# Performance work log

Measured on AMD Instinct MI355X. Metric: run time of the kernel, lower is better.

Reference implementation:

```python
import jax, jax.numpy as jnp
import numpy as np
from jax import lax

S = 20      # max_segments
D = 1000    # traj_dict entries
L = 200     # dmp_traj_length
CONV_OUT = 512 * 4 * 4  # 8192 for 100x100 input


def _conv(x, w, b):
    # NCHW valid conv, kernel 3x3, stride 1 (matches nn.Conv2d defaults)
    y = lax.conv_general_dilated(x, w, (1, 1), 'VALID',
                                 dimension_numbers=('NCHW', 'OIHW', 'NCHW'))
    return y + b[None, :, None, None]


def _pool2(x):
    # max_pool2d(kernel=2, stride=2), floor mode == VALID reduce_window
    return lax.reduce_window(x, -jnp.inf, lax.max, (1, 1, 2, 2), (1, 1, 2, 2), 'VALID')


def setup_inputs() -> dict:
    key = jax.random.key(0)
    ks = jax.random.split(key, 20)
    f32 = jnp.float32

    def rn(k, shape, s):
        return jax.random.normal(k, shape, dtype=f32) * s

    x = jax.random.normal(ks[0], (128, 3, 100, 100), dtype=f32)
    w1 = rn(ks[1], (64, 3, 3, 3), 0.1);    b1 = jnp.zeros((64,), f32)
    w2 = rn(ks[2], (128, 64, 3, 3), 0.04); b2 = jnp.zeros((128,), f32)
    w3 = rn(ks[3], (256, 128, 3, 3), 0.03); b3 = jnp.zeros((256,), f32)
    w4 = rn(ks[4], (512, 256, 3, 3), 0.02); b4 = jnp.zeros((512,), f32)
    out_size = 2 + 3 * S
    fw1 = rn(ks[5], (CONV_OUT, 2048), 0.01); fb1 = jnp.zeros((2048,), f32)
    fw2 = rn(ks[6], (2048, 2048), 0.02);     fb2 = jnp.zeros((2048,), f32)
    fw3 = rn(ks[7], (2048, out_size), 0.02); fb3 = jnp.zeros((out_size,), f32)
    traj_dict = jax.random.normal(ks[8], (D, L, 2), dtype=f32)
    return {
        'x': x,
        'w1': w1, 'b1': b1, 'w2': w2, 'b2': b2,
        'w3': w3, 'b3': b3, 'w4': w4, 'b4': b4,
        'fw1': fw1, 'fb1': fb1, 'fw2': fw2, 'fb2': fb2,
        'fw3': fw3, 'fb3': fb3,
        'traj_dict': traj_dict,
    }


def _forward(x, w1, b1, w2, b2, w3, b3, w4, b4,
             fw1, fb1, fw2, fb2, fw3, fb3, traj_dict):
    # conv encoder (relu(maxpool(conv)) x4, matching the torch order)
    h = jax.nn.relu(_pool2(_conv(x, w1, b1)))
    h = jax.nn.relu(_pool2(_conv(h, w2, b2)))
    h = jax.nn.relu(_pool2(_conv(h, w3, b3)))
    h = jax.nn.relu(_pool2(_conv(h, w4, b4)))
    h = h.reshape(h.shape[0], -1)                      # [B, 8192]
    # FC stack: tanh on hidden layers, linear head (dropout p=0 / eval)
    h = jnp.tanh(h @ fw1 + fb1)
    h = jnp.tanh(h @ fw2 + fb2)
    p = h @ fw3 + fb3                                  # [B, 2 + 3S]

    B = p.shape[0]
    init_pos = p[:, :2]                                # [B, 2]
    seg = p[:, 2:].reshape(B, S, 3)                    # (dict_idx, x_scale, y_scale)

    # getTrajFromDict: the loop of round/clamp/sign/abs one-hot masks is exactly
    # a gather at the clamped rounded index (round is half-to-even in both torch and jax)
    idx = jnp.clip(jnp.round(seg[..., 0]), 0, D - 1).astype(jnp.int32)  # [B, S]
    base = traj_dict[idx]                              # [B, S, L, 2]

    scaled = base * seg[:, :, None, 1:3]               # [B, S, L, 2]
    # chain segments: each segment starts at previous segment's endpoint
    offsets = scaled[:, :, -1, :]                      # [B, S, 2]
    starts = init_pos[:, None, :] + jnp.cumsum(offsets, axis=1) - offsets  # exclusive cumsum
    traj = (scaled + starts[:, :, None, :]).reshape(B, S * L, 2)
    return traj


def reference(x, w1, b1, w2, b2, w3, b3, w4, b4,
              fw1, fb1, fw2, fb2, fw3, fb3, traj_dict):
    return _forward(x, w1, b1, w2, b2, w3, b3, w4, b4,
                    fw1, fb1, fw2, fb2, fw3, fb3, traj_dict)
```

## Files before the change

kernel.cpp:

```cpp
#include <hip/hip_runtime.h>
#include <hip/hip_bf16.h>

typedef __attribute__((ext_vector_type(8))) short s8v;
typedef __attribute__((ext_vector_type(4))) float f4v;
typedef unsigned short ushort;
typedef unsigned int uint;

union V8 { s8v v; short s[8]; };

__device__ __forceinline__ short f2bf(float v){
    union { __hip_bfloat16 b; short u; } x;
    x.b = __float2bfloat16(v);
    return x.u;
}
__device__ __forceinline__ float bf2f(short u){
    union { short u; __hip_bfloat16 b; } x;
    x.u = u;
    return __bfloat162float(x.b);
}
__device__ __forceinline__ void splitf(float v, short& h, short& l){
    h = f2bf(v);
    l = f2bf(v - bf2f(h));
}
__device__ __forceinline__ uint packsplit(float v){
    short h, l; splitf(v, h, l);
    return (uint)(ushort)h | ((uint)(ushort)l << 16);
}

template<int CIN, int HIN, int PH, int OCB, int SPT, int CICH, int COUT>
__global__ __launch_bounds__(SPT) void k_conv_pool_relu(
    const float* __restrict__ in, const float* __restrict__ w,
    const float* __restrict__ bias, uint* __restrict__ out)
{
    constexpr int WIN   = HIN;
    constexpr int PW    = PH;
    constexpr int WSTR  = CICH * 9 + 1;

    __shared__ float wsh[OCB * WSTR];

    const int b   = blockIdx.z;
    const int oc0 = blockIdx.y * OCB;
    const int t   = threadIdx.x;
    const int sp  = blockIdx.x * SPT + t;
    const bool active = sp < PH * PW;
    const int py = active ? (sp / PW) : 0;
    const int px = active ? (sp % PW) : 0;

    float acc[OCB][4];
#pragma unroll
    for (int j = 0; j < OCB; ++j)
        acc[j][0] = acc[j][1] = acc[j][2] = acc[j][3] = 0.f;

    const float* inb = in + (size_t)b * CIN * HIN * WIN;

    for (int c0 = 0; c0 < CIN; c0 += CICH) {
        __syncthreads();
        for (int i = t; i < OCB * CICH * 9; i += SPT) {
            int j = i / (CICH * 9);
            int r = i - j * (CICH * 9);
            wsh[j * WSTR + r] = w[((size_t)(oc0 + j) * CIN + c0) * 9 + r];
        }
        __syncthreads();

        for (int ci = 0; ci < CICH; ++ci) {
            const float* inc = inb + (size_t)(c0 + ci) * HIN * WIN
                             + (2 * py) * WIN + 2 * px;
            float patch[4][4];
#pragma unroll
            for (int r = 0; r < 4; ++r)
#pragma unroll
                for (int c = 0; c < 4; ++c)
                    patch[r][c] = inc[r * WIN + c];

#pragma unroll
            for (int j = 0; j < OCB; ++j) {
                const float* wp = &wsh[j * WSTR + ci * 9];
#pragma unroll
                for (int kh = 0; kh < 3; ++kh)
#pragma unroll
                    for (int kw = 0; kw < 3; ++kw) {
                        float wv = wp[kh * 3 + kw];
                        acc[j][0] = fmaf(patch[kh][kw],         wv, acc[j][0]);
                        acc[j][1] = fmaf(patch[kh][kw + 1],     wv, acc[j][1]);
                        acc[j][2] = fmaf(patch[kh + 1][kw],     wv, acc[j][2]);
                        acc[j][3] = fmaf(patch[kh + 1][kw + 1], wv, acc[j][3]);
                    }
            }
        }
    }

    if (active) {
        uint tmp[OCB];
#pragma unroll
        for (int j = 0; j < OCB; ++j) {
            float m = fmaxf(fmaxf(acc[j][0], acc[j][1]),
                            fmaxf(acc[j][2], acc[j][3]));
            m = fmaxf(m + bias[oc0 + j], 0.f);
            tmp[j] = packsplit(m);
        }
        uint* ob = out + ((size_t)b * PH * PW + sp) * COUT + oc0;
#pragma unroll
        for (int q = 0; q < OCB / 4; ++q)
            ((uint4*)ob)[q] = ((const uint4*)tmp)[q];
    }
}

__global__ void k_wsplit_perm(const float* __restrict__ w, ushort* __restrict__ oh,
                              ushort* __restrict__ ol, int CIN, int total)
{
    int i = blockIdx.x * 256 + threadIdx.x;
    if (i < total) {
        int K = CIN * 9;
        int n = i / K;
        int rem = i - n * K;
        int ci = rem / 9;
        int r = rem - 9 * ci;
        short h, l; splitf(w[i], h, l);
        size_t o = (size_t)n * K + r * CIN + ci;
        oh[o] = (ushort)h; ol[o] = (ushort)l;
    }
}

__global__ __launch_bounds__(256) void k_wsplitT(
    const float* __restrict__ B, ushort* __restrict__ oh, ushort* __restrict__ ol,
    int K, int N)
{
    __shared__ float tl[32][33];
    const int n0 = blockIdx.x * 32, k0 = blockIdx.y * 32;
    const int r = threadIdx.x >> 5, c = threadIdx.x & 31;
#pragma unroll
    for (int it = 0; it < 4; ++it) {
        int row = r + it * 8;
        tl[row][c] = B[(size_t)(k0 + row) * N + n0 + c];
    }
    __syncthreads();
#pragma unroll
    for (int it = 0; it < 4; ++it) {
        int a = r + it * 8;
        float v = tl[c][a];
        short h, l; splitf(v, h, l);
        size_t o = (size_t)(n0 + a) * K + k0 + c;
        oh[o] = (ushort)h; ol[o] = (ushort)l;
    }
}

template<int MODE, int BPRE, int EPI, int LOG2CIN, int K, int KCH, int N,
         int HIN, int PPH, int PPW, int COUT, int TPI, int MT>
__global__ __launch_bounds__(256) void k_gemm4(
    const void* __restrict__ A0, const void* __restrict__ A1,
    const void* __restrict__ B0, const void* __restrict__ B1,
    const float* __restrict__ bias, void* __restrict__ O0, void* __restrict__ O1)
{
    constexpr int CIN  = 1 << LOG2CIN;
    constexpr int HH   = HIN * HIN;
    constexpr int WM   = MT / 32;
    constexpr int AOPT = MT / 64;
    constexpr int OSTEP = 256 / MT;

    __shared__ short Ah[MT][40], Al[MT][40], Bh[128][40], Bl[128][40];

    const int t    = threadIdx.x;
    const int lane = t & 63;
    const int wave = t >> 6;
    const int n0   = blockIdx.y * 128;
    const int sArow = t & (MT - 1), sAo0 = t / MT;
    const int sBrow = t & 127, sBo = t >> 7;

    const uint*   ArI = nullptr;
    const ushort* Ahg = nullptr;
    const ushort* Alg = nullptr;
    int b = 0, ptile = 0, kbeg = 0, kend = K;

    if (MODE == 0) {
        b = blockIdx.x / TPI;
        ptile = blockIdx.x - b * TPI;
        int pl = ptile * (MT / 4) + (sArow >> 2);
        int quad = sArow & 3;
        int py = 0, px = 0;
        if (pl < PPH * PPW) { py = pl / PPW; px = pl - py * PPW; }
        ArI = (const uint*)A0
            + ((size_t)b * HH + (size_t)(2 * py + (quad >> 1)) * HIN
               + (2 * px + (quad & 1))) * CIN;
    } else {
        int arow = blockIdx.x * MT + sArow;
        Ahg = (const ushort*)A0 + (size_t)arow * K;
        Alg = (const ushort*)A1 + (size_t)arow * K;
        kbeg = blockIdx.z * KCH;
        kend = kbeg + KCH;
    }

    auto pfA = [&](int kkx, V8* ha, V8* la) {
#pragma unroll
        for (int q = 0; q < AOPT; ++q) {
            const int kb = kkx + (sAo0 + q * OSTEP) * 8;
            if (MODE == 0) {
                const int r  = kb >> LOG2CIN;
                const int cb = kb & (CIN - 1);
                const int rh = (r * 11) >> 5;
                const int rw = r - 3 * rh;
                const uint* g = ArI + (rh * HIN + rw) * CIN + cb;
                uint4 v0 = *(const uint4*)g;
                uint4 v1 = *(const uint4*)(g + 4);
                uint vv[8] = {v0.x, v0.y, v0.z, v0.w, v1.x, v1.y, v1.z, v1.w};
#pragma unroll
                for (int j = 0; j < 8; ++j) {
                    ha[q].s[j] = (short)(vv[j] & 0xffffu);
                    la[q].s[j] = (short)(vv[j] >> 16);
                }
            } else {
                ha[q].v = *(const s8v*)(Ahg + kb);
                la[q].v = *(const s8v*)(Alg + kb);
            }
        }
    };
    auto pfB = [&](int kkx, V8* hb, V8* lb) {
#pragma unroll
        for (int q = 0; q < 2; ++q) {
            const int o = sBo + 2 * q;
            const int kb = kkx + o * 8;
            if (BPRE) {
                hb[q].v = *(const s8v*)((const ushort*)B0 + (size_t)(n0 + sBrow) * K + kb);
                lb[q].v = *(const s8v*)((const ushort*)B1 + (size_t)(n0 + sBrow) * K + kb);
            } else if (MODE == 0) {
                const int r  = kb >> LOG2CIN;
                const int cb = kb & (CIN - 1);
                const float* bp = (const float*)B0
                    + (size_t)(n0 + sBrow) * K + (size_t)cb * 9 + r;
#pragma unroll
                for (int j = 0; j < 8; ++j)
                    splitf(bp[9 * j], hb[q].s[j], lb[q].s[j]);
            } else {
                const float* bp = (const float*)B0 + (size_t)kb * N + n0 + sBrow;
#pragma unroll
                for (int j = 0; j < 8; ++j)
                    splitf(bp[(size_t)j * N], hb[q].s[j], lb[q].s[j]);
            }
        }
    };

    f4v acc[WM][4];
    const f4v z4 = {0.f, 0.f, 0.f, 0.f};
#pragma unroll
    for (int i = 0; i < WM; ++i)
#pragma unroll
        for (int j = 0; j < 4; ++j) acc[i][j] = z4;

    V8 pAh[AOPT], pAl[AOPT], pBh[2], pBl[2];
    pfA(kbeg, pAh, pAl);
    pfB(kbeg, pBh, pBl);

    for (int kk = kbeg; kk < kend; kk += 32) {
        __syncthreads();
#pragma unroll
        for (int q = 0; q < AOPT; ++q) {
            const int o = sAo0 + q * OSTEP;
            *(s8v*)&Ah[sArow][o * 8] = pAh[q].v;
            *(s8v*)&Al[sArow][o * 8] = pAl[q].v;
        }
#pragma unroll
        for (int q = 0; q < 2; ++q) {
            const int o = sBo + 2 * q;
            *(s8v*)&Bh[sBrow][o * 8] = pBh[q].v;
            *(s8v*)&Bl[sBrow][o * 8] = pBl[q].v;
        }
        if (kk + 32 < kend) {
            pfA(kk + 32, pAh, pAl);
            pfB(kk + 32, pBh, pBl);
        }
        __syncthreads();

        const int fm = lane & 15;
        const int fk = (lane >> 4) * 8;
        s8v a_h[WM], a_l[WM], b_h[4], b_l[4];
#pragma unroll
        for (int i = 0; i < WM; ++i) {
            a_h[i] = *(const s8v*)&Ah[(wave & 1) * (MT / 2) + i * 16 + fm][fk];
            a_l[i] = *(const s8v*)&Al[(wave & 1) * (MT / 2) + i * 16 + fm][fk];
        }
#pragma unroll
        for (int j = 0; j < 4; ++j) {
            b_h[j] = *(const s8v*)&Bh[(wave >> 1) * 64 + j * 16 + fm][fk];
            b_l[j] = *(const s8v*)&Bl[(wave >> 1) * 64 + j * 16 + fm][fk];
        }
#define MF(a_, b_, c_) c_ = __builtin_amdgcn_mfma_f32_16x16x32_bf16(a_, b_, c_, 0, 0, 0)
#pragma unroll
        for (int i = 0; i < WM; ++i)
#pragma unroll
            for (int j = 0; j < 4; ++j) {
                MF(a_h[i], b_h[j], acc[i][j]);
                MF(a_h[i], b_l[j], acc[i][j]);
                MF(a_l[i], b_h[j], acc[i][j]);
            }
#undef MF
    }

    if (MODE == 0) {
        const int PP = PPH * PPW;
#pragma unroll
        for (int i = 0; i < WM; ++i)
#pragma unroll
            for (int j = 0; j < 4; ++j) {
                int p  = ptile * (MT / 4) + (wave & 1) * (MT / 8) + i * 4 + (lane >> 4);
                int oc = n0 + (wave >> 1) * 64 + j * 16 + (lane & 15);
                if (p < PP) {
                    f4v v = acc[i][j];
                    float m = fmaxf(fmaxf(v.x, v.y), fmaxf(v.z, v.w));
                    m = fmaxf(m + bias[oc], 0.f);
                    if (EPI == 0) {
                        ((uint*)O0)[((size_t)b * PP + p) * COUT + oc] = packsplit(m);
                    } else {
                        size_t o = (size_t)(b * COUT + oc) * PP + p;
                        short h, l; splitf(m, h, l);
                        ((ushort*)O0)[o] = (ushort)h;
                        ((ushort*)O1)[o] = (ushort)l;
                    }
                }
            }
    } else {
        float* P = (float*)O0 + (size_t)blockIdx.z * 128 * N;
#pragma unroll
        for (int i = 0; i < WM; ++i)
#pragma unroll
            for (int j = 0; j < 4; ++j) {
                int n = n0 + (wave >> 1) * 64 + j * 16 + (lane & 15);
                int mb = blockIdx.x * MT + (wave & 1) * (MT / 2) + i * 16 + (lane >> 4) * 4;
                f4v v = acc[i][j];
                P[(size_t)(mb + 0) * N + n] = v.x;
                P[(size_t)(mb + 1) * N + n] = v.y;
                P[(size_t)(mb + 2) * N + n] = v.z;
                P[(size_t)(mb + 3) * N + n] = v.w;
            }
    }
}

template<int EFMT>
__global__ void k_fc_epi2(const float* __restrict__ P, const float* __restrict__ bias,
                          ushort* __restrict__ oh, ushort* __restrict__ ol,
                          float* __restrict__ of, int MN, int N, int KS)
{
    int i = blockIdx.x * 256 + threadIdx.x;
    if (i >= MN) return;
    float s = 0.f;
    for (int z = 0; z < KS; ++z) s += P[(size_t)z * MN + i];
    s = tanhf(s + bias[i % N]);
    if (EFMT == 1) {
        short h, l; splitf(s, h, l);
        oh[i] = (ushort)h; ol[i] = (ushort)l;
    } else {
        of[i] = s;
    }
}

__global__ __launch_bounds__(64) void k_fc3_part(
    const float* __restrict__ A, const float* __restrict__ B,
    float* __restrict__ P, int K, int N, int KS)
{
    const int m = blockIdx.x, kz = blockIdx.y;
    const int n = threadIdx.x;
    const int kchunk = K / KS;
    if (n < N) {
        float acc = 0.f;
        const float* Am = A + (size_t)m * K;
        const int ke = (kz + 1) * kchunk;
        for (int k = kz * kchunk; k < ke; ++k)
            acc = fmaf(Am[k], B[(size_t)k * N + n], acc);
        P[((size_t)kz * 128 + m) * N + n] = acc;
    }
}

__global__ void k_fc_epi(const float* __restrict__ P, const float* __restrict__ bias,
                         float* __restrict__ out, int MN, int N, int KS)
{
    int i = blockIdx.x * 256 + threadIdx.x;
    if (i >= MN) return;
    float s = 0.f;
    for (int z = 0; z < KS; ++z) s += P[(size_t)z * MN + i];
    out[i] = s + bias[i % N];
}

__global__ void k_traj_start(const float* __restrict__ p, const float* __restrict__ td,
                             float* __restrict__ starts, float* __restrict__ sa,
                             int* __restrict__ sidx)
{
    int b = threadIdx.x;
    const float* pb = p + b * 62;
    float cx = pb[0], cy = pb[1];
    for (int s = 0; s < 20; ++s) {
        float f  = pb[2 + 3 * s];
        float a0 = pb[3 + 3 * s];
        float a1 = pb[4 + 3 * s];
        int idx = (int)fminf(fmaxf(rintf(f), 0.f), 999.f);
        int bs = b * 20 + s;
        sidx[bs] = idx;
        sa[bs * 2 + 0] = a0;
        sa[bs * 2 + 1] = a1;
        starts[bs * 2 + 0] = cx;
        starts[bs * 2 + 1] = cy;
        cx += td[((size_t)idx * 200 + 199) * 2 + 0] * a0;
        cy += td[((size_t)idx * 200 + 199) * 2 + 1] * a1;
    }
}

__global__ void k_traj_main(const float* __restrict__ td, const float* __restrict__ starts,
                            const float* __restrict__ sa, const int* __restrict__ sidx,
                            float* __restrict__ out)
{
    int bs = blockIdx.x;
    int idx = sidx[bs];
    float a0 = sa[bs * 2 + 0], a1 = sa[bs * 2 + 1];
    float s0 = starts[bs * 2 + 0], s1 = starts[bs * 2 + 1];
    const float* row = td + (size_t)idx * 400;
    float* o = out + (size_t)bs * 400;
    for (int e = threadIdx.x; e < 400; e += blockDim.x) {
        float v = row[e];
        o[e] = (e & 1) ? fmaf(v, a1, s1) : fmaf(v, a0, s0);
    }
}

template<int BPRE>
static void run_all(void* const* d_in, float* out, char* ws, hipStream_t stream)
{
    const float* x   = (const float*)d_in[0];
    const float* w1  = (const float*)d_in[1];
    const float* b1  = (const float*)d_in[2];
    const float* w2  = (const float*)d_in[3];
    const float* b2  = (const float*)d_in[4];
    const float* w3  = (const float*)d_in[5];
    const float* b3  = (const float*)d_in[6];
    const float* w4  = (const float*)d_in[7];
    const float* b4  = (const float*)d_in[8];
    const float* fw1 = (const float*)d_in[9];
    const float* fb1 = (const float*)d_in[10];
    const float* fw2 = (const float*)d_in[11];
    const float* fb2 = (const float*)d_in[12];
    const float* fw3 = (const float*)d_in[13];
    const float* fb3 = (const float*)d_in[14];
    const float* td  = (const float*)d_in[15];

    uint*   h1   = (uint*)ws;
    uint*   h2   = (uint*)(ws + 78675968ull);
    uint*   h3   = (uint*)ws;
    ushort* fw1h = (ushort*)(ws + 13107200ull);
    ushort* fw1l = (ushort*)(ws + 46661632ull);
    ushort* h4h  = (ushort*)(ws + 80216064ull);
    ushort* h4l  = (ushort*)(ws + 82313216ull);
    ushort* fw2h = (ushort*)(ws + 84410368ull);
    ushort* fw2l = (ushort*)(ws + 92798976ull);
    float*  part = (float*)(ws + 101187584ull);
    ushort* a1h  = (ushort*)(ws + 109576192ull);
    ushort* a1l  = (ushort*)(ws + 110100480ull);
    float*  a2   = (float*)(ws + 110624768ull);
    float*  p    = (float*)(ws + 111673344ull);
    float*  starts = (float*)(ws + 111705088ull);
    float*  sa   = (float*)(ws + 111725568ull);
    int*    sidx = (int*)(ws + 111746048ull);
    ushort* w2h = (ushort*)(ws + 113344512ull);
    ushort* w2l = (ushort*)(ws + 113491968ull);
    ushort* w3h = (ushort*)(ws + 113639424ull);
    ushort* w3l = (ushort*)(ws + 114229248ull);
    ushort* w4h = (ushort*)(ws + 114819072ull);
    ushort* w4l = (ushort*)(ws + 117178368ull);

    if (BPRE) {
        k_wsplit_perm<<<(73728 + 255) / 256, 256, 0, stream>>>(w2, w2h, w2l, 64, 73728);
        k_wsplit_perm<<<(294912 + 255) / 256, 256, 0, stream>>>(w3, w3h, w3l, 128, 294912);
        k_wsplit_perm<<<(1179648 + 255) / 256, 256, 0, stream>>>(w4, w4h, w4l, 256, 1179648);
    }

    k_conv_pool_relu<3, 100, 49, 16, 256, 3, 64>
        <<<dim3(10, 4, 128), 256, 0, stream>>>(x, w1, b1, h1);

    k_gemm4<0, BPRE, 0, 6, 576, 576, 128, 49, 23, 23, 128, 17, 128>
        <<<dim3(17 * 128, 1), 256, 0, stream>>>(
            h1, nullptr, BPRE ? (const void*)w2h : (const void*)w2,
            BPRE ? (const void*)w2l : nullptr, b2, h2, nullptr);
    k_gemm4<0, BPRE, 0, 7, 1152, 1152, 256, 23, 10, 10, 256, 4, 128>
        <<<dim3(4 * 128, 2), 256, 0, stream>>>(
            h2, nullptr, BPRE ? (const void*)w3h : (const void*)w3,
            BPRE ? (const void*)w3l : nullptr, b3, h3, nullptr);

    if (BPRE) {
        k_wsplitT<<<dim3(2048 / 32, 8192 / 32), 256, 0, stream>>>(fw1, fw1h, fw1l, 8192, 2048);
        k_wsplitT<<<dim3(2048 / 32, 2048 / 32), 256, 0, stream>>>(fw2, fw2h, fw2l, 2048, 2048);
    }

    k_gemm4<0, BPRE, 1, 8, 2304, 2304, 512, 10, 4, 4, 512, 1, 64>
        <<<dim3(128, 4), 256, 0, stream>>>(
            h3, nullptr, BPRE ? (const void*)w4h : (const void*)w4,
            BPRE ? (const void*)w4l : nullptr, b4, h4h, h4l);

    k_gemm4<1, BPRE, 2, 0, 8192, 1024, 2048, 1, 1, 1, 1, 1, 64>
        <<<dim3(2, 16, 8), 256, 0, stream>>>(
            h4h, h4l, BPRE ? (const void*)fw1h : (const void*)fw1,
            BPRE ? (const void*)fw1l : nullptr, nullptr, part, nullptr);
    k_fc_epi2<1><<<(128 * 2048 + 255) / 256, 256, 0, stream>>>(
        part, fb1, a1h, a1l, nullptr, 128 * 2048, 2048, 8);
    k_gemm4<1, BPRE, 2, 0, 2048, 256, 2048, 1, 1, 1, 1, 1, 64>
        <<<dim3(2, 16, 8), 256, 0, stream>>>(
            a1h, a1l, BPRE ? (const void*)fw2h : (const void*)fw2,
            BPRE ? (const void*)fw2l : nullptr, nullptr, part, nullptr);
    k_fc_epi2<2><<<(128 * 2048 + 255) / 256, 256, 0, stream>>>(
        part, fb2, nullptr, nullptr, a2, 128 * 2048, 2048, 8);

    k_fc3_part<<<dim3(128, 4), 64, 0, stream>>>(a2, fw3, part, 2048, 62, 4);
    k_fc_epi<<<(128 * 62 + 255) / 256, 256, 0, stream>>>(
        part, fb3, p, 128 * 62, 62, 4);
    k_traj_start<<<1, 128, 0, stream>>>(p, td, starts, sa, sidx);
    k_traj_main<<<2560, 256, 0, stream>>>(td, starts, sa, sidx, out);
}

extern "C" void kernel_launch(void* const* d_in, const int* in_sizes, int n_in,
                              void* d_out, int out_size, void* d_ws, size_t ws_size,
                              hipStream_t stream)
{
    (void)in_sizes; (void)n_in; (void)out_size;
    if (ws_size >= 119537664ull)
        run_all<1>(d_in, (float*)d_out, (char*)d_ws, stream);
    else
        run_all<0>(d_in, (float*)d_out, (char*)d_ws, stream);
}
```

Baseline: 948.6 us.

## Stage GEMM tiles via global_load_lds and split activations into hi/lo planes

Stores intermediate activations as separate bf16 hi and lo planes instead of packed uint pairs, so GEMM A operands can be copied with 16-byte direct global-to-LDS loads. The register-prefetch double buffer is replaced by per-iteration global_load_lds staging into a k-major LDS layout with no padding. This cuts VGPR use and unpacking work, but it drops the overlap between the next tile's loads and the current tile's MFMAs, and the unpadded layout may cause LDS bank conflicts.

```diff
diff --git a/kernel.cpp b/kernel.cpp
--- a/kernel.cpp
+++ b/kernel.cpp
@@ -22,15 +22,18 @@
     h = f2bf(v);
     l = f2bf(v - bf2f(h));
 }
-__device__ __forceinline__ uint packsplit(float v){
-    short h, l; splitf(v, h, l);
-    return (uint)(ushort)h | ((uint)(ushort)l << 16);
+
+__device__ __forceinline__ void gl_lds16(const void* g, void* l){
+    __builtin_amdgcn_global_load_lds(
+        (const __attribute__((address_space(1))) void*)g,
+        (__attribute__((address_space(3))) void*)l, 16, 0, 0);
 }
 
 template<int CIN, int HIN, int PH, int OCB, int SPT, int CICH, int COUT>
 __global__ __launch_bounds__(SPT) void k_conv_pool_relu(
     const float* __restrict__ in, const float* __restrict__ w,
-    const float* __restrict__ bias, uint* __restrict__ out)
+    const float* __restrict__ bias, ushort* __restrict__ outh,
+    ushort* __restrict__ outl)
 {
     constexpr int WIN   = HIN;
     constexpr int PW    = PH;
@@ -90,18 +93,21 @@
     }
 
     if (active) {
-        uint tmp[OCB];
+        union { ushort us[OCB]; uint4 u4[OCB / 8]; } TH, TL;
 #pragma unroll
         for (int j = 0; j < OCB; ++j) {
             float m = fmaxf(fmaxf(acc[j][0], acc[j][1]),
                             fmaxf(acc[j][2], acc[j][3]));
             m = fmaxf(m + bias[oc0 + j], 0.f);
-            tmp[j] = packsplit(m);
-        }
-        uint* ob = out + ((size_t)b * PH * PW + sp) * COUT + oc0;
-#pragma unroll
-        for (int q = 0; q < OCB / 4; ++q)
-            ((uint4*)ob)[q] = ((const uint4*)tmp)[q];
+            short h, l; splitf(m, h, l);
+            TH.us[j] = (ushort)h; TL.us[j] = (ushort)l;
+        }
+        size_t base = ((size_t)b * PH * PW + sp) * COUT + oc0;
+#pragma unroll
+        for (int q = 0; q < OCB / 8; ++q) {
+            ((uint4*)(outh + base))[q] = TH.u4[q];
+            ((uint4*)(outl + base))[q] = TL.u4[q];
+        }
     }
 }
 
@@ -157,7 +163,8 @@
     constexpr int AOPT = MT / 64;
     constexpr int OSTEP = 256 / MT;
 
-    __shared__ short Ah[MT][40], Al[MT][40], Bh[128][40], Bl[128][40];
+    __shared__ ushort Ah[4][MT][8], Al[4][MT][8];
+    __shared__ ushort Bh[4][128][8], Bl[4][128][8];
 
     const int t    = threadIdx.x;
     const int lane = t & 63;
@@ -165,8 +172,12 @@
     const int n0   = blockIdx.y * 128;
     const int sArow = t & (MT - 1), sAo0 = t / MT;
     const int sBrow = t & 127, sBo = t >> 7;
-
-    const uint*   ArI = nullptr;
+    const int rbA = sArow - lane;
+    const int rbB = sBrow - lane;
+
+    const ushort* Ahp = (const ushort*)A0;
+    const ushort* Alp = (const ushort*)A1;
+    size_t aoff = 0;
     const ushort* Ahg = nullptr;
     const ushort* Alg = nullptr;
     int b = 0, ptile = 0, kbeg = 0, kend = K;
@@ -178,8 +189,7 @@
         int quad = sArow & 3;
         int py = 0, px = 0;
         if (pl < PPH * PPW) { py = pl / PPW; px = pl - py * PPW; }
-        ArI = (const uint*)A0
-            + ((size_t)b * HH + (size_t)(2 * py + (quad >> 1)) * HIN
+        aoff = ((size_t)b * HH + (size_t)(2 * py + (quad >> 1)) * HIN
                + (2 * px + (quad & 1))) * CIN;
     } else {
         int arow = blockIdx.x * MT + sArow;
@@ -189,51 +199,55 @@
         kend = kbeg + KCH;
     }
 
-    auto pfA = [&](int kkx, V8* ha, V8* la) {
+    auto stage = [&](int kkx) {
 #pragma unroll
         for (int q = 0; q < AOPT; ++q) {
-            const int kb = kkx + (sAo0 + q * OSTEP) * 8;
+            const int ko = sAo0 + q * OSTEP;
+            const int kb = kkx + ko * 8;
             if (MODE == 0) {
                 const int r  = kb >> LOG2CIN;
                 const int cb = kb & (CIN - 1);
                 const int rh = (r * 11) >> 5;
                 const int rw = r - 3 * rh;
-                const uint* g = ArI + (rh * HIN + rw) * CIN + cb;
-                uint4 v0 = *(const uint4*)g;
-                uint4 v1 = *(const uint4*)(g + 4);
-                uint vv[8] = {v0.x, v0.y, v0.z, v0.w, v1.x, v1.y, v1.z, v1.w};
-#pragma unroll
-                for (int j = 0; j < 8; ++j) {
-                    ha[q].s[j] = (short)(vv[j] & 0xffffu);
-                    la[q].s[j] = (short)(vv[j] >> 16);
+                const size_t g = aoff + (size_t)(rh * HIN + rw) * CIN + cb;
+                gl_lds16(Ahp + g, &Ah[ko][rbA][0]);
+                gl_lds16(Alp + g, &Al[ko][rbA][0]);
+            } else {
+                gl_lds16(Ahg + kb, &Ah[ko][rbA][0]);
+                gl_lds16(Alg + kb, &Al[ko][rbA][0]);
+            }
+        }
+        if (BPRE) {
+#pragma unroll
+            for (int q = 0; q < 2; ++q) {
+                const int o = sBo + 2 * q;
+                const int kb = kkx + o * 8;
+                const size_t g = (size_t)(n0 + sBrow) * K + kb;
+                gl_lds16((const ushort*)B0 + g, &Bh[o][rbB][0]);
+                gl_lds16((const ushort*)B1 + g, &Bl[o][rbB][0]);
+            }
+        } else {
+#pragma unroll
+            for (int q = 0; q < 2; ++q) {
+                const int o = sBo + 2 * q;
+                const int kb = kkx + o * 8;
+                V8 hb, lb;
+                if (MODE == 0) {
+                    const int r  = kb >> LOG2CIN;
+                    const int cb = kb & (CIN - 1);
+                    const float* bp = (const float*)B0
+                        + (size_t)(n0 + sBrow) * K + (size_t)cb * 9 + r;
+#pragma unroll
+                    for (int j = 0; j < 8; ++j)
+                        splitf(bp[9 * j], hb.s[j], lb.s[j]);
+                } else {
+                    const float* bp = (const float*)B0 + (size_t)kb * N + n0 + sBrow;
+#pragma unroll
+                    for (int j = 0; j < 8; ++j)
+                        splitf(bp[(size_t)j * N], hb.s[j], lb.s[j]);
                 }
-            } else {
-                ha[q].v = *(const s8v*)(Ahg + kb);
-                la[q].v = *(const s8v*)(Alg + kb);
-            }
-        }
-    };
-    auto pfB = [&](int kkx, V8* hb, V8* lb) {
-#pragma unroll
-        for (int q = 0; q < 2; ++q) {
-            const int o = sBo + 2 * q;
-            const int kb = kkx + o * 8;
-            if (BPRE) {
-                hb[q].v = *(const s8v*)((const ushort*)B0 + (size_t)(n0 + sBrow) * K + kb);
-                lb[q].v = *(const s8v*)((const ushort*)B1 + (size_t)(n0 + sBrow) * K + kb);
-            } else if (MODE == 0) {
-                const int r  = kb >> LOG2CIN;
-                const int cb = kb & (CIN - 1);
-                const float* bp = (const float*)B0
-                    + (size_t)(n0 + sBrow) * K + (size_t)cb * 9 + r;
-#pragma unroll
-                for (int j = 0; j < 8; ++j)
-                    splitf(bp[9 * j], hb[q].s[j], lb[q].s[j]);
-            } else {
-                const float* bp = (const float*)B0 + (size_t)kb * N + n0 + sBrow;
-#pragma unroll
-                for (int j = 0; j < 8; ++j)
-                    splitf(bp[(size_t)j * N], hb[q].s[j], lb[q].s[j]);
+                *(s8v*)&Bh[o][sBrow][0] = hb.v;
+                *(s8v*)&Bl[o][sBrow][0] = lb.v;
             }
         }
     };
@@ -245,42 +259,21 @@
 #pragma unroll
         for (int j = 0; j < 4; ++j) acc[i][j] = z4;
 
-    V8 pAh[AOPT], pAl[AOPT], pBh[2], pBl[2];
-    pfA(kbeg, pAh, pAl);
-    pfB(kbeg, pBh, pBl);
-
     for (int kk = kbeg; kk < kend; kk += 32) {
+        stage(kk);
         __syncthreads();
-#pragma unroll
-        for (int q = 0; q < AOPT; ++q) {
-            const int o = sAo0 + q * OSTEP;
-            *(s8v*)&Ah[sArow][o * 8] = pAh[q].v;
-            *(s8v*)&Al[sArow][o * 8] = pAl[q].v;
-        }
-#pragma unroll
-        for (int q = 0; q < 2; ++q) {
-            const int o = sBo + 2 * q;
-            *(s8v*)&Bh[sBrow][o * 8] = pBh[q].v;
-            *(s8v*)&Bl[sBrow][o * 8] = pBl[q].v;
-        }
-        if (kk + 32 < kend) {
-            pfA(kk + 32, pAh, pAl);
-            pfB(kk + 32, pBh, pBl);
-        }
-        __syncthreads();
-
         const int fm = lane & 15;
-        const int fk = (lane >> 4) * 8;
+        const int ko = lane >> 4;
         s8v a_h[WM], a_l[WM], b_h[4], b_l[4];
 #pragma unroll
         for (int i = 0; i < WM; ++i) {
-            a_h[i] = *(const s8v*)&Ah[(wave & 1) * (MT / 2) + i * 16 + fm][fk];
-            a_l[i] = *(const s8v*)&Al[(wave & 1) * (MT / 2) + i * 16 + fm][fk];
+            a_h[i] = *(const s8v*)&Ah[ko][(wave & 1) * (MT / 2) + i * 16 + fm][0];
+            a_l[i] = *(const s8v*)&Al[ko][(wave & 1) * (MT / 2) + i * 16 + fm][0];
         }
 #pragma unroll
         for (int j = 0; j < 4; ++j) {
-            b_h[j] = *(const s8v*)&Bh[(wave >> 1) * 64 + j * 16 + fm][fk];
-            b_l[j] = *(const s8v*)&Bl[(wave >> 1) * 64 + j * 16 + fm][fk];
+            b_h[j] = *(const s8v*)&Bh[ko][(wave >> 1) * 64 + j * 16 + fm][0];
+            b_l[j] = *(const s8v*)&Bl[ko][(wave >> 1) * 64 + j * 16 + fm][0];
         }
 #define MF(a_, b_, c_) c_ = __builtin_amdgcn_mfma_f32_16x16x32_bf16(a_, b_, c_, 0, 0, 0)
 #pragma unroll
@@ -292,6 +285,7 @@
                 MF(a_l[i], b_h[j], acc[i][j]);
             }
 #undef MF
+        __syncthreads();
     }
 
     if (MODE == 0) {
@@ -306,11 +300,13 @@
                     f4v v = acc[i][j];
                     float m = fmaxf(fmaxf(v.x, v.y), fmaxf(v.z, v.w));
                     m = fmaxf(m + bias[oc], 0.f);
+                    short h, l; splitf(m, h, l);
                     if (EPI == 0) {
-                        ((uint*)O0)[((size_t)b * PP + p) * COUT + oc] = packsplit(m);
+                        size_t o = ((size_t)b * PP + p) * COUT + oc;
+                        ((ushort*)O0)[o] = (ushort)h;
+                        ((ushort*)O1)[o] = (ushort)l;
                     } else {
                         size_t o = (size_t)(b * COUT + oc) * PP + p;
-                        short h, l; splitf(m, h, l);
                         ((ushort*)O0)[o] = (ushort)h;
                         ((ushort*)O1)[o] = (ushort)l;
                     }
@@ -437,9 +433,12 @@
     const float* fb3 = (const float*)d_in[14];
     const float* td  = (const float*)d_in[15];
 
-    uint*   h1   = (uint*)ws;
-    uint*   h2   = (uint*)(ws + 78675968ull);
-    uint*   h3   = (uint*)ws;
+    ushort* h1h  = (ushort*)ws;
+    ushort* h1l  = (ushort*)(ws + 39337984ull);
+    ushort* h2h  = (ushort*)(ws + 78675968ull);
+    ushort* h2l  = (ushort*)(ws + 96010240ull);
+    ushort* h3h  = (ushort*)ws;
+    ushort* h3l  = (ushort*)(ws + 6553600ull);
     ushort* fw1h = (ushort*)(ws + 13107200ull);
     ushort* fw1l = (ushort*)(ws + 46661632ull);
     ushort* h4h  = (ushort*)(ws + 80216064ull);
@@ -468,16 +467,16 @@
     }
 
     k_conv_pool_relu<3, 100, 49, 16, 256, 3, 64>
-        <<<dim3(10, 4, 128), 256, 0, stream>>>(x, w1, b1, h1);
+        <<<dim3(10, 4, 128), 256, 0, stream>>>(x, w1, b1, h1h, h1l);
 
     k_gemm4<0, BPRE, 0, 6, 576, 576, 128, 49, 23, 23, 128, 17, 128>
         <<<dim3(17 * 128, 1), 256, 0, stream>>>(
-            h1, nullptr, BPRE ? (const void*)w2h : (const void*)w2,
-            BPRE ? (const void*)w2l : nullptr, b2, h2, nullptr);
+            h1h, h1l, BPRE ? (const void*)w2h : (const void*)w2,
+            BPRE ? (const void*)w2l : nullptr, b2, h2h, h2l);
     k_gemm4<0, BPRE, 0, 7, 1152, 1152, 256, 23, 10, 10, 256, 4, 128>
         <<<dim3(4 * 128, 2), 256, 0, stream>>>(
-            h2, nullptr, BPRE ? (const void*)w3h : (const void*)w3,
-            BPRE ? (const void*)w3l : nullptr, b3, h3, nullptr);
+            h2h, h2l, BPRE ? (const void*)w3h : (const void*)w3,
+            BPRE ? (const void*)w3l : nullptr, b3, h3h, h3l);
 
     if (BPRE) {
         k_wsplitT<<<dim3(2048 / 32, 8192 / 32), 256, 0, stream>>>(fw1, fw1h, fw1l, 8192, 2048);
@@ -486,7 +485,7 @@
 
     k_gemm4<0, BPRE, 1, 8, 2304, 2304, 512, 10, 4, 4, 512, 1, 64>
         <<<dim3(128, 4), 256, 0, stream>>>(
-            h3, nullptr, BPRE ? (const void*)w4h : (const void*)w4,
+            h3h, h3l, BPRE ? (const void*)w4h : (const void*)w4,
             BPRE ? (const void*)w4l : nullptr, b4, h4h, h4l);
 
     k_gemm4<1, BPRE, 2, 0, 8192, 1024, 2048, 1, 1, 1, 1, 1, 64>
```

After: 1.000 ms. 1.05x slower.
